# Optimization experiments

Hardware: AMD Instinct MI355X
Metric: run time of the kernel (lower is better)

Reference implementation:

```python
import jax, jax.numpy as jnp
import numpy as np

N_NODES = 50000


def sage_conv(x, src, dst, W_l, W_r, b):
    # mean-aggregate neighbor features: out_i = W_l @ mean_{j->i} x_j + W_r @ x_i + b
    msg_sum = jax.ops.segment_sum(x[src], dst, num_segments=N_NODES)   # [N, F]
    cnt = jax.ops.segment_sum(jnp.ones_like(dst, dtype=x.dtype), dst, num_segments=N_NODES)
    mean = msg_sum / jnp.maximum(cnt, 1.0)[:, None]                    # zero for isolated nodes
    return mean @ W_l + x @ W_r + b


def setup_inputs() -> dict:
    key = jax.random.key(0)
    ks = jax.random.split(key, 8)
    in_dim, hid, out_dim = 128, 128, 128
    x = jax.random.normal(ks[0], (N_NODES, in_dim), dtype=jnp.float32)
    edge_index = jax.random.randint(ks[1], (2, 800000), 0, N_NODES, dtype=jnp.int64)
    s0 = 1.0 / np.sqrt(in_dim)
    s1 = 1.0 / np.sqrt(hid)
    return {
        "x": x,
        "edge_index": edge_index,
        "W_l0": jax.random.uniform(ks[2], (in_dim, hid), jnp.float32, -s0, s0),
        "W_r0": jax.random.uniform(ks[3], (in_dim, hid), jnp.float32, -s0, s0),
        "b0": jnp.zeros((hid,), jnp.float32),
        "W_l1": jax.random.uniform(ks[4], (hid, out_dim), jnp.float32, -s1, s1),
        "W_r1": jax.random.uniform(ks[5], (hid, out_dim), jnp.float32, -s1, s1),
        "b1": jnp.zeros((out_dim,), jnp.float32),
    }


def reference(x, edge_index, W_l0, W_r0, b0, W_l1, W_r1, b1):
    src, dst = edge_index[0], edge_index[1]
    h = sage_conv(x, src, dst, W_l0, W_r0, b0)
    h = jax.nn.relu(h)
    out = sage_conv(h, src, dst, W_l1, W_r1, b1)
    return out
```

## Files before the change

### kernel.cpp

```cpp
#include <hip/hip_runtime.h>

#define FDIM 128
#define NGRP 8

typedef __attribute__((ext_vector_type(4))) float f32x4;
typedef __attribute__((ext_vector_type(8))) short s16x8;
typedef __attribute__((ext_vector_type(4))) short s16x4;

__device__ inline unsigned short f2bf(float f) {
    unsigned u = __builtin_bit_cast(unsigned, f);
    u += 0x7FFFu + ((u >> 16) & 1u);
    return (unsigned short)(u >> 16);
}
__device__ inline float bflo(unsigned u) { return __builtin_bit_cast(float, u << 16); }
__device__ inline float bfhi(unsigned u) { return __builtin_bit_cast(float, u & 0xFFFF0000u); }

__global__ void prologue_kernel(int4* __restrict__ degg4, int nz,
                                const float* __restrict__ x, short* __restrict__ xb, int n4x,
                                const float* __restrict__ Wl0, const float* __restrict__ Wr0,
                                const float* __restrict__ Wl1, const float* __restrict__ Wr1,
                                short* __restrict__ Wt0, short* __restrict__ Wt1,
                                int ZB, int XB) {
    int bid = blockIdx.x;
    if (bid < ZB) {
        int i = bid * 256 + threadIdx.x;
        if (i < nz) degg4[i] = make_int4(0, 0, 0, 0);
    } else if (bid < ZB + XB) {
        int i = (bid - ZB) * 256 + threadIdx.x;
        if (i < n4x) {
            float4 v = reinterpret_cast<const float4*>(x)[i];
            s16x4 o;
            o[0] = (short)f2bf(v.x); o[1] = (short)f2bf(v.y);
            o[2] = (short)f2bf(v.z); o[3] = (short)f2bf(v.w);
            reinterpret_cast<s16x4*>(xb)[i] = o;
        }
    } else {
        int g = (bid - ZB - XB) * 256 + threadIdx.x;
        int n = g & 127;
        int k = (g >> 7) & 255;
        int layer = g >> 15;
        const float* Wl = layer ? Wl1 : Wl0;
        const float* Wr = layer ? Wr1 : Wr0;
        short* Wt = layer ? Wt1 : Wt0;
        float v = (k < 128) ? Wl[k * 128 + n] : Wr[(k - 128) * 128 + n];
        Wt[n * 256 + k] = (short)f2bf(v);
    }
}

__global__ void hist8_kernel(const int* __restrict__ dst, int* __restrict__ degg, int E, int N) {
    int e = blockIdx.x * blockDim.x + threadIdx.x;
    if (e < E) atomicAdd(&degg[(blockIdx.x & 7) * N + dst[e]], 1);
}

__global__ void scanA1_kernel(const int* __restrict__ in, int* __restrict__ out,
                              int* __restrict__ bsum, int M) {
    __shared__ int s[256];
    int base = blockIdx.x * 1024 + threadIdx.x * 4;
    int4 v = make_int4(0, 0, 0, 0);
    if (base + 3 < M) v = *reinterpret_cast<const int4*>(in + base);
    else {
        if (base + 0 < M) v.x = in[base + 0];
        if (base + 1 < M) v.y = in[base + 1];
        if (base + 2 < M) v.z = in[base + 2];
        if (base + 3 < M) v.w = in[base + 3];
    }
    int tsum = v.x + v.y + v.z + v.w;
    s[threadIdx.x] = tsum;
    __syncthreads();
    for (int off = 1; off < 256; off <<= 1) {
        int t = (threadIdx.x >= off) ? s[threadIdx.x - off] : 0;
        __syncthreads();
        s[threadIdx.x] += t;
        __syncthreads();
    }
    int excl = s[threadIdx.x] - tsum;
    int4 o;
    o.x = excl; o.y = excl + v.x; o.z = o.y + v.y; o.w = o.z + v.z;
    if (base + 3 < M) *reinterpret_cast<int4*>(out + base) = o;
    else {
        if (base + 0 < M) out[base + 0] = o.x;
        if (base + 1 < M) out[base + 1] = o.y;
        if (base + 2 < M) out[base + 2] = o.z;
    }
    if (threadIdx.x == 255) bsum[blockIdx.x] = s[255];
}

__global__ void scanA3_kernel(int* __restrict__ off, int* __restrict__ cursor,
                              const int* __restrict__ bsum, int nb, int M, int E) {
    __shared__ int s[256];
    int t = threadIdx.x;
    int v = 0;
    if (t < blockIdx.x) v += bsum[t];
    if (t + 256 < blockIdx.x) v += bsum[t + 256];
    s[t] = v;
    __syncthreads();
    for (int off2 = 128; off2 > 0; off2 >>= 1) {
        if (t < off2) s[t] += s[t + off2];
        __syncthreads();
    }
    int b = s[0];

    int base = blockIdx.x * 1024 + t * 4;
    if (base + 3 < M) {
        int4 w = *reinterpret_cast<const int4*>(off + base);
        w.x += b; w.y += b; w.z += b; w.w += b;
        *reinterpret_cast<int4*>(off + base) = w;
        *reinterpret_cast<int4*>(cursor + base) = w;
    } else {
#pragma unroll
        for (int j = 0; j < 4; ++j)
            if (base + j < M) { int q = off[base + j] + b; off[base + j] = q; cursor[base + j] = q; }
    }
    if (base == 0) off[M] = E;
}

__global__ void rp_kernel(const int* __restrict__ off, int* __restrict__ rp, int N, int E) {
    __shared__ int S0;
    if (threadIdx.x == 0) {
        int s = 0;
#pragma unroll
        for (int g = 0; g < NGRP; ++g) s += off[g * N];
        S0 = s;
    }
    __syncthreads();
    int i = blockIdx.x * 256 + threadIdx.x;
    if (i < N) {
        int s = 0;
#pragma unroll
        for (int g = 0; g < NGRP; ++g) s += off[g * N + i];
        rp[i] = s - S0;
    } else if (i == N) {
        rp[N] = E;
    }
}

__global__ void fill8_kernel(const int* __restrict__ src, const int* __restrict__ dst,
                             int* __restrict__ cursor, int* __restrict__ eidt, int E, int N) {
    int e = blockIdx.x * blockDim.x + threadIdx.x;
    if (e < E) {
        int p = atomicAdd(&cursor[(blockIdx.x & 7) * N + dst[e]], 1);
        eidt[p] = src[e];
    }
}

__global__ void merge_kernel(const int* __restrict__ off, const int* __restrict__ eidt,
                             const int* __restrict__ rp, int* __restrict__ eid, int N) {
    int i = blockIdx.x * 256 + threadIdx.x;
    if (i >= N) return;
    int dp = rp[i];
#pragma unroll
    for (int g = 0; g < NGRP; ++g) {
        int b = off[g * N + i];
        int e2 = off[g * N + i + 1];
        for (int k = b; k < e2; ++k) eid[dp++] = eidt[k];
    }
}

#define ACC8(v) { a[0]+=bflo(v.x); a[1]+=bfhi(v.x); a[2]+=bflo(v.y); a[3]+=bfhi(v.y); \
                  a[4]+=bflo(v.z); a[5]+=bfhi(v.z); a[6]+=bflo(v.w); a[7]+=bfhi(v.w); }

__global__ void gather_kernel(const short* __restrict__ X, const int* __restrict__ rp,
                              const int* __restrict__ eid, short* __restrict__ mb, int N) {
    int node = blockIdx.x * (blockDim.x >> 6) + (threadIdx.x >> 6);
    int lane = threadIdx.x & 63;
    int g = lane >> 4;
    int c = lane & 15;
    if (node >= N) return;
    int beg = rp[node], end = rp[node + 1];
    float a[8];
#pragma unroll
    for (int j = 0; j < 8; ++j) a[j] = 0.0f;

    int k = beg;
    for (; k + 16 <= end; k += 16) {
        int s0 = eid[k + g];
        int s1 = eid[k + 4 + g];
        int s2 = eid[k + 8 + g];
        int s3 = eid[k + 12 + g];
        uint4 v0 = *reinterpret_cast<const uint4*>(X + (size_t)s0 * FDIM + c * 8);
        uint4 v1 = *reinterpret_cast<const uint4*>(X + (size_t)s1 * FDIM + c * 8);
        uint4 v2 = *reinterpret_cast<const uint4*>(X + (size_t)s2 * FDIM + c * 8);
        uint4 v3 = *reinterpret_cast<const uint4*>(X + (size_t)s3 * FDIM + c * 8);
        ACC8(v0); ACC8(v1); ACC8(v2); ACC8(v3);
    }
    if (k + 8 <= end) {
        int s0 = eid[k + g];
        int s1 = eid[k + 4 + g];
        uint4 v0 = *reinterpret_cast<const uint4*>(X + (size_t)s0 * FDIM + c * 8);
        uint4 v1 = *reinterpret_cast<const uint4*>(X + (size_t)s1 * FDIM + c * 8);
        ACC8(v0); ACC8(v1);
        k += 8;
    }
    if (k + 4 <= end) {
        int s0 = eid[k + g];
        uint4 v0 = *reinterpret_cast<const uint4*>(X + (size_t)s0 * FDIM + c * 8);
        ACC8(v0);
        k += 4;
    }
    int rem = end - k;
    if (g < rem) {
        int s0 = eid[k + g];
        uint4 v0 = *reinterpret_cast<const uint4*>(X + (size_t)s0 * FDIM + c * 8);
        ACC8(v0);
    }

#pragma unroll
    for (int j = 0; j < 8; ++j) a[j] += __shfl_xor(a[j], 16);
#pragma unroll
    for (int j = 0; j < 8; ++j) a[j] += __shfl_xor(a[j], 32);

    if (g == 0) {
        float inv = (end > beg) ? 1.0f / (float)(end - beg) : 0.0f;
        uint4 o;
        o.x = (unsigned)f2bf(a[0] * inv) | ((unsigned)f2bf(a[1] * inv) << 16);
        o.y = (unsigned)f2bf(a[2] * inv) | ((unsigned)f2bf(a[3] * inv) << 16);
        o.z = (unsigned)f2bf(a[4] * inv) | ((unsigned)f2bf(a[5] * inv) << 16);
        o.w = (unsigned)f2bf(a[6] * inv) | ((unsigned)f2bf(a[7] * inv) << 16);
        *reinterpret_cast<uint4*>(mb + (size_t)node * FDIM + c * 8) = o;
    }
}

template <bool RELU, bool OUTF32>
__global__ __launch_bounds__(256, 3)
void gemm_mfma_kernel(const short* __restrict__ Am, const short* Ax,
                      const short* __restrict__ Wt, const float* __restrict__ bias,
                      float* outf, short* outb, int n) {
    __shared__ short A_lds[64 * 256];
    const int tid = threadIdx.x;
    const int w = tid >> 6, l = tid & 63;
    const int row0 = blockIdx.x * 64;

    s16x8 bfr[8][2];
    {
        const short* wb = Wt + ((32 * w + (l & 15)) * 256 + 8 * (l >> 4));
#pragma unroll
        for (int kc = 0; kc < 8; ++kc)
#pragma unroll
            for (int cf = 0; cf < 2; ++cf)
                bfr[kc][cf] = *reinterpret_cast<const s16x8*>(wb + cf * 16 * 256 + kc * 32);
    }

#pragma unroll
    for (int i = 0; i < 8; ++i) {
        int c = tid + 256 * i;
        int r = c >> 5;
        int ck = c & 31;
        int row = row0 + r;
        s16x8 v;
        if (row < n) {
            const short* sp = (ck < 16) ? (Am + (size_t)row * FDIM + ck * 8)
                                        : (Ax + (size_t)row * FDIM + (ck - 16) * 8);
            v = *reinterpret_cast<const s16x8*>(sp);
        } else {
#pragma unroll
            for (int j = 0; j < 8; ++j) v[j] = 0;
        }
        int byte = r * 512 + ((ck * 16) ^ ((r & 7) << 4));
        *reinterpret_cast<s16x8*>(reinterpret_cast<char*>(A_lds) + byte) = v;
    }
    __syncthreads();

    f32x4 acc[4][2];
    {
        float b0 = bias[32 * w + (l & 15)];
        float b1 = bias[32 * w + 16 + (l & 15)];
#pragma unroll
        for (int rf = 0; rf < 4; ++rf)
#pragma unroll
            for (int i = 0; i < 4; ++i) { acc[rf][0][i] = b0; acc[rf][1][i] = b1; }
    }

    const int arow = l & 15;
    const int aq16 = 16 * (l >> 4);
#pragma unroll
    for (int kc = 0; kc < 8; ++kc) {
        s16x8 afr[4];
#pragma unroll
        for (int rf = 0; rf < 4; ++rf) {
            int r = 16 * rf + arow;
            int kbyte = 64 * kc + aq16;
            int byte = r * 512 + (kbyte ^ ((r & 7) << 4));
            afr[rf] = *reinterpret_cast<const s16x8*>(reinterpret_cast<const char*>(A_lds) + byte);
        }
#pragma unroll
        for (int rf = 0; rf < 4; ++rf)
#pragma unroll
            for (int cf = 0; cf < 2; ++cf)
                acc[rf][cf] = __builtin_amdgcn_mfma_f32_16x16x32_bf16(afr[rf], bfr[kc][cf], acc[rf][cf], 0, 0, 0);
    }

    const int ocol = 32 * w + (l & 15);
    const int orow = 4 * (l >> 4);
#pragma unroll
    for (int rf = 0; rf < 4; ++rf)
#pragma unroll
        for (int cf = 0; cf < 2; ++cf)
#pragma unroll
            for (int i = 0; i < 4; ++i) {
                int row = row0 + 16 * rf + orow + i;
                if (row < n) {
                    float v = acc[rf][cf][i];
                    if (RELU) v = fmaxf(v, 0.0f);
                    if (OUTF32) outf[(size_t)row * FDIM + ocol + 16 * cf] = v;
                    else        outb[(size_t)row * FDIM + ocol + 16 * cf] = (short)f2bf(v);
                }
            }
}

__global__ void degree_kernel(const int* __restrict__ dst, float* __restrict__ cnt, int E) {
    int e = blockIdx.x * blockDim.x + threadIdx.x;
    if (e < E) atomicAdd(&cnt[dst[e]], 1.0f);
}

__global__ void scatter_kernel(const float* __restrict__ x, const int* __restrict__ src,
                               const int* __restrict__ dst, float* __restrict__ msg, int E) {
    int gt = blockIdx.x * blockDim.x + threadIdx.x;
    int e = gt >> 6;
    int lane = gt & 63;
    if (e >= E) return;
    int s = src[e];
    int d = dst[e];
    float2 v = reinterpret_cast<const float2*>(x + (size_t)s * FDIM)[lane];
    float* md = msg + (size_t)d * FDIM + 2 * lane;
    atomicAdd(md, v.x);
    atomicAdd(md + 1, v.y);
}

template <bool RELU>
__global__ void gemm_kernel(const float* agg, const float* cnt,
                            const float* __restrict__ xin, const float* __restrict__ Wl,
                            const float* __restrict__ Wr, const float* __restrict__ bias,
                            float* out, int n) {
    const int ROWS = 16;
    __shared__ float m_s[ROWS][FDIM];
    __shared__ float x_s[ROWS][FDIM];
    int tid = threadIdx.x;
    int row0 = blockIdx.x * ROWS;
#pragma unroll
    for (int i = 0; i < 2; ++i) {
        int idx4 = tid + i * 256;
        int r = idx4 >> 5;
        int c4 = idx4 & 31;
        int row = row0 + r;
        if (row < n) {
            float inv = cnt ? 1.0f / fmaxf(cnt[row], 1.0f) : 1.0f;
            float4 mv = reinterpret_cast<const float4*>(agg + (size_t)row * FDIM)[c4];
            float4 xv = reinterpret_cast<const float4*>(xin + (size_t)row * FDIM)[c4];
            float* mp = &m_s[r][c4 * 4];
            mp[0] = mv.x * inv; mp[1] = mv.y * inv; mp[2] = mv.z * inv; mp[3] = mv.w * inv;
            float* xp = &x_s[r][c4 * 4];
            xp[0] = xv.x; xp[1] = xv.y; xp[2] = xv.z; xp[3] = xv.w;
        }
    }
    __syncthreads();
    int j = tid & 127;
    int rh = tid >> 7;
    float acc[8];
    float bj = bias[j];
#pragma unroll
    for (int r = 0; r < 8; ++r) acc[r] = bj;
#pragma unroll 4
    for (int k = 0; k < FDIM; ++k) {
        float wl = Wl[k * FDIM + j];
        float wr = Wr[k * FDIM + j];
#pragma unroll
        for (int r = 0; r < 8; ++r)
            acc[r] += m_s[rh * 8 + r][k] * wl + x_s[rh * 8 + r][k] * wr;
    }
#pragma unroll
    for (int r = 0; r < 8; ++r) {
        int row = row0 + rh * 8 + r;
        if (row < n) {
            float v = acc[r];
            if (RELU) v = fmaxf(v, 0.0f);
            out[(size_t)row * FDIM + j] = v;
        }
    }
}

extern "C" void kernel_launch(void* const* d_in, const int* in_sizes, int n_in,
                              void* d_out, int out_size, void* d_ws, size_t ws_size,
                              hipStream_t stream) {
    const float* x   = (const float*)d_in[0];
    const int*   ei  = (const int*)d_in[1];
    const float* Wl0 = (const float*)d_in[2];
    const float* Wr0 = (const float*)d_in[3];
    const float* b0  = (const float*)d_in[4];
    const float* Wl1 = (const float*)d_in[5];
    const float* Wr1 = (const float*)d_in[6];
    const float* b1  = (const float*)d_in[7];

    int N = in_sizes[0] / FDIM;
    int E = in_sizes[1] / 2;
    const int* src = ei;
    const int* dst = ei + E;

    size_t featBytes  = (size_t)N * FDIM * sizeof(float);
    size_t featBytesB = (size_t)N * FDIM * sizeof(short);
    int edgeBlocks = (E + 255) / 256;
    int M = NGRP * N;
    int blocksA = (M + 1023) / 1024;

    const size_t o_bsum = 0x0;
    const size_t o_rp   = 0x1000;
    const size_t o_wt0  = 0x33000;
    const size_t o_wt1  = 0x43000;
    const size_t o_eid  = 0x53000;
    const size_t o_xb   = 0x361000;
    const size_t o_mb   = o_xb + featBytesB;
    const size_t need   = o_mb + featBytesB;
    const size_t s_degg = o_mb + 0x0;
    const size_t s_off  = o_mb + 0x187000;
    const size_t s_cur  = o_mb + 0x30E000;
    const size_t s_eidt = o_mb + 0x495000;

    if (ws_size >= need && blocksA <= 512) {
        int*   bsum   = (int*)((char*)d_ws + o_bsum);
        int*   rp     = (int*)((char*)d_ws + o_rp);
        short* Wt0    = (short*)((char*)d_ws + o_wt0);
        short* Wt1    = (short*)((char*)d_ws + o_wt1);
        int*   eid    = (int*)((char*)d_ws + o_eid);
        short* xb     = (short*)((char*)d_ws + o_xb);
        short* mb     = (short*)((char*)d_ws + o_mb);
        int*   degg   = (int*)((char*)d_ws + s_degg);
        int*   off    = (int*)((char*)d_ws + s_off);
        int*   cursor = (int*)((char*)d_ws + s_cur);
        int*   eidt   = (int*)((char*)d_ws + s_eidt);
        float* outF   = (float*)d_out;

        int nz  = M / 4;
        int n4x = N * FDIM / 4;
        int ZB = (nz + 255) / 256;
        int XB = (n4x + 255) / 256;
        int WB = (65536 + 255) / 256;
        prologue_kernel<<<ZB + XB + WB, 256, 0, stream>>>(
            (int4*)degg, nz, x, xb, n4x, Wl0, Wr0, Wl1, Wr1, Wt0, Wt1, ZB, XB);

        hist8_kernel<<<edgeBlocks, 256, 0, stream>>>(dst, degg, E, N);
        scanA1_kernel<<<blocksA, 256, 0, stream>>>(degg, off, bsum, M);
        scanA3_kernel<<<blocksA, 256, 0, stream>>>(off, cursor, bsum, blocksA, M, E);
        rp_kernel<<<(N + 256) / 256, 256, 0, stream>>>(off, rp, N, E);
        fill8_kernel<<<edgeBlocks, 256, 0, stream>>>(src, dst, cursor, eidt, E, N);
        merge_kernel<<<(N + 255) / 256, 256, 0, stream>>>(off, eidt, rp, eid, N);

        int gatherBlocks = (N + 3) / 4;
        int gemmBlocks   = (N + 63) / 64;
        gather_kernel<<<gatherBlocks, 256, 0, stream>>>(xb, rp, eid, mb, N);
        gemm_mfma_kernel<true, false><<<gemmBlocks, 256, 0, stream>>>(mb, xb, Wt0, b0, nullptr, xb, N);
        gather_kernel<<<gatherBlocks, 256, 0, stream>>>(xb, rp, eid, mb, N);
        gemm_mfma_kernel<false, true><<<gemmBlocks, 256, 0, stream>>>(mb, xb, Wt1, b1, outF, nullptr, N);
    } else {
        float* cnt = (float*)d_ws;
        float* h   = (float*)((char*)d_ws + (1 << 18));
        float* msg = (float*)d_out;
        int gemmBlocks = (N + 15) / 16;

        hipMemsetAsync(cnt, 0, (size_t)N * sizeof(float), stream);
        degree_kernel<<<edgeBlocks, 256, 0, stream>>>(dst, cnt, E);

        hipMemsetAsync(msg, 0, featBytes, stream);
        scatter_kernel<<<(E * 64 + 255) / 256, 256, 0, stream>>>(x, src, dst, msg, E);
        gemm_kernel<true><<<gemmBlocks, 256, 0, stream>>>(msg, cnt, x, Wl0, Wr0, b0, h, N);

        hipMemsetAsync(msg, 0, featBytes, stream);
        scatter_kernel<<<(E * 64 + 255) / 256, 256, 0, stream>>>(h, src, dst, msg, E);
        gemm_kernel<false><<<gemmBlocks, 256, 0, stream>>>(msg, cnt, h, Wl1, Wr1, b1, msg, N);
    }
}
```

Before: 188.5 us.

## Fuse CSR build into fewer launches with a decoupled look-back single-pass scan

Replaces the two-pass block scan (scanA1 + scanA3) with a single-pass decoupled look-back scan that uses per-block status flags in the workspace. It folds the row-pointer computation into the merge kernel, and co-schedules the weight transpose with the histogram and the x-to-bf16 conversion with the fill kernel. This cuts the launch count in the preprocessing chain and lets independent work overlap the atomic-bound kernels. The look-back spins on flags and assumes earlier blocks make forward progress; the zero kernel must also clear the state array.

```diff
diff --git a/kernel.cpp b/kernel.cpp
--- a/kernel.cpp
+++ b/kernel.cpp
@@ -15,27 +15,21 @@
 __device__ inline float bflo(unsigned u) { return __builtin_bit_cast(float, u << 16); }
 __device__ inline float bfhi(unsigned u) { return __builtin_bit_cast(float, u & 0xFFFF0000u); }
 
-__global__ void prologue_kernel(int4* __restrict__ degg4, int nz,
-                                const float* __restrict__ x, short* __restrict__ xb, int n4x,
-                                const float* __restrict__ Wl0, const float* __restrict__ Wr0,
-                                const float* __restrict__ Wl1, const float* __restrict__ Wr1,
-                                short* __restrict__ Wt0, short* __restrict__ Wt1,
-                                int ZB, int XB) {
+__global__ void zero_kernel(int4* __restrict__ p, int n4) {
+    int i = blockIdx.x * blockDim.x + threadIdx.x;
+    if (i < n4) p[i] = make_int4(0, 0, 0, 0);
+}
+
+__global__ void hist8w_kernel(const int* __restrict__ dst, int* __restrict__ degg, int E, int N, int EB,
+                              const float* __restrict__ Wl0, const float* __restrict__ Wr0,
+                              const float* __restrict__ Wl1, const float* __restrict__ Wr1,
+                              short* __restrict__ Wt0, short* __restrict__ Wt1) {
     int bid = blockIdx.x;
-    if (bid < ZB) {
-        int i = bid * 256 + threadIdx.x;
-        if (i < nz) degg4[i] = make_int4(0, 0, 0, 0);
-    } else if (bid < ZB + XB) {
-        int i = (bid - ZB) * 256 + threadIdx.x;
-        if (i < n4x) {
-            float4 v = reinterpret_cast<const float4*>(x)[i];
-            s16x4 o;
-            o[0] = (short)f2bf(v.x); o[1] = (short)f2bf(v.y);
-            o[2] = (short)f2bf(v.z); o[3] = (short)f2bf(v.w);
-            reinterpret_cast<s16x4*>(xb)[i] = o;
-        }
+    if (bid < EB) {
+        int e = bid * 256 + threadIdx.x;
+        if (e < E) atomicAdd(&degg[(bid & 7) * N + dst[e]], 1);
     } else {
-        int g = (bid - ZB - XB) * 256 + threadIdx.x;
+        int g = (bid - EB) * 256 + threadIdx.x;
         int n = g & 127;
         int k = (g >> 7) & 255;
         int layer = g >> 15;
@@ -47,74 +41,112 @@
     }
 }
 
-__global__ void hist8_kernel(const int* __restrict__ dst, int* __restrict__ degg, int E, int N) {
-    int e = blockIdx.x * blockDim.x + threadIdx.x;
-    if (e < E) atomicAdd(&degg[(blockIdx.x & 7) * N + dst[e]], 1);
-}
-
-__global__ void scanA1_kernel(const int* __restrict__ in, int* __restrict__ out,
-                              int* __restrict__ bsum, int M) {
+__global__ __launch_bounds__(256)
+void scan_kernel(const int* __restrict__ in, int* __restrict__ out, int* __restrict__ cursor,
+                 unsigned* __restrict__ state, int M, int E) {
     __shared__ int s[256];
-    int base = blockIdx.x * 1024 + threadIdx.x * 4;
+    __shared__ int s_excl;
+    const int bid = blockIdx.x;
+    const int t = threadIdx.x;
+    int base = bid * 1024 + t * 4;
     int4 v = make_int4(0, 0, 0, 0);
     if (base + 3 < M) v = *reinterpret_cast<const int4*>(in + base);
     else {
         if (base + 0 < M) v.x = in[base + 0];
         if (base + 1 < M) v.y = in[base + 1];
         if (base + 2 < M) v.z = in[base + 2];
-        if (base + 3 < M) v.w = in[base + 3];
     }
     int tsum = v.x + v.y + v.z + v.w;
-    s[threadIdx.x] = tsum;
+    s[t] = tsum;
     __syncthreads();
-    for (int off = 1; off < 256; off <<= 1) {
-        int t = (threadIdx.x >= off) ? s[threadIdx.x - off] : 0;
+    for (int o2 = 1; o2 < 256; o2 <<= 1) {
+        int tt = (t >= o2) ? s[t - o2] : 0;
         __syncthreads();
-        s[threadIdx.x] += t;
+        s[t] += tt;
         __syncthreads();
     }
-    int excl = s[threadIdx.x] - tsum;
+    int total = s[255];
+    int texcl = s[t] - tsum;
+
+    if (t == 0) {
+        unsigned w = ((bid == 0 ? 2u : 1u) << 30) | (unsigned)total;
+        __hip_atomic_store(&state[bid], w, __ATOMIC_RELEASE, __HIP_MEMORY_SCOPE_AGENT);
+    }
+    if (t < 64) {
+        int excl = 0;
+        int j = bid - 1;
+        while (j >= 0) {
+            int idx = j - t;
+            unsigned w = 0;
+            if (idx >= 0) {
+                do {
+                    w = __hip_atomic_load(&state[idx], __ATOMIC_ACQUIRE, __HIP_MEMORY_SCOPE_AGENT);
+                } while ((w >> 30) == 0u);
+            }
+            int val = (int)(w & 0x3FFFFFFFu);
+            bool isPre = (idx >= 0) && ((w >> 30) == 2u);
+            unsigned long long mask = __ballot(isPre);
+            int contrib;
+            if (mask) {
+                int stop = __ffsll((unsigned long long)mask) - 1;
+                contrib = (t <= stop) ? val : 0;
+            } else {
+                contrib = (idx >= 0) ? val : 0;
+            }
+            for (int o = 32; o > 0; o >>= 1) contrib += __shfl_down(contrib, o);
+            excl += contrib;
+            if (mask) break;
+            j -= 64;
+        }
+        if (t == 0) {
+            s_excl = excl;
+            unsigned w = (2u << 30) | (unsigned)(excl + total);
+            __hip_atomic_store(&state[bid], w, __ATOMIC_RELEASE, __HIP_MEMORY_SCOPE_AGENT);
+        }
+    }
+    __syncthreads();
+    int b = s_excl;
+
+    int e0 = b + texcl;
     int4 o;
-    o.x = excl; o.y = excl + v.x; o.z = o.y + v.y; o.w = o.z + v.z;
-    if (base + 3 < M) *reinterpret_cast<int4*>(out + base) = o;
-    else {
-        if (base + 0 < M) out[base + 0] = o.x;
-        if (base + 1 < M) out[base + 1] = o.y;
-        if (base + 2 < M) out[base + 2] = o.z;
-    }
-    if (threadIdx.x == 255) bsum[blockIdx.x] = s[255];
-}
-
-__global__ void scanA3_kernel(int* __restrict__ off, int* __restrict__ cursor,
-                              const int* __restrict__ bsum, int nb, int M, int E) {
-    __shared__ int s[256];
-    int t = threadIdx.x;
-    int v = 0;
-    if (t < blockIdx.x) v += bsum[t];
-    if (t + 256 < blockIdx.x) v += bsum[t + 256];
-    s[t] = v;
-    __syncthreads();
-    for (int off2 = 128; off2 > 0; off2 >>= 1) {
-        if (t < off2) s[t] += s[t + off2];
-        __syncthreads();
-    }
-    int b = s[0];
-
-    int base = blockIdx.x * 1024 + t * 4;
+    o.x = e0; o.y = o.x + v.x; o.z = o.y + v.y; o.w = o.z + v.z;
     if (base + 3 < M) {
-        int4 w = *reinterpret_cast<const int4*>(off + base);
-        w.x += b; w.y += b; w.z += b; w.w += b;
-        *reinterpret_cast<int4*>(off + base) = w;
-        *reinterpret_cast<int4*>(cursor + base) = w;
+        *reinterpret_cast<int4*>(out + base) = o;
+        *reinterpret_cast<int4*>(cursor + base) = o;
     } else {
 #pragma unroll
-        for (int j = 0; j < 4; ++j)
-            if (base + j < M) { int q = off[base + j] + b; off[base + j] = q; cursor[base + j] = q; }
-    }
-    if (base == 0) off[M] = E;
-}
-
-__global__ void rp_kernel(const int* __restrict__ off, int* __restrict__ rp, int N, int E) {
+        for (int j2 = 0; j2 < 3; ++j2) {
+            int vv = (j2 == 0) ? o.x : (j2 == 1) ? o.y : o.z;
+            if (base + j2 < M) { out[base + j2] = vv; cursor[base + j2] = vv; }
+        }
+    }
+    if (bid == 0 && t == 0) out[M] = E;
+}
+
+__global__ void fill8x_kernel(const int* __restrict__ src, const int* __restrict__ dst,
+                              int* __restrict__ cursor, int* __restrict__ eidt, int E, int N, int EB,
+                              const float* __restrict__ x, short* __restrict__ xb, int n4x) {
+    int bid = blockIdx.x;
+    if (bid < EB) {
+        int e = bid * 256 + threadIdx.x;
+        if (e < E) {
+            int p = atomicAdd(&cursor[(bid & 7) * N + dst[e]], 1);
+            eidt[p] = src[e];
+        }
+    } else {
+        int i = (bid - EB) * 256 + threadIdx.x;
+        if (i < n4x) {
+            float4 v = reinterpret_cast<const float4*>(x)[i];
+            s16x4 o;
+            o[0] = (short)f2bf(v.x); o[1] = (short)f2bf(v.y);
+            o[2] = (short)f2bf(v.z); o[3] = (short)f2bf(v.w);
+            reinterpret_cast<s16x4*>(xb)[i] = o;
+        }
+    }
+}
+
+__global__ void merge_kernel(const int* __restrict__ off, const int* __restrict__ eidt,
+                             int* __restrict__ rp, int* __restrict__ eid, int N, int E) {
     __shared__ int S0;
     if (threadIdx.x == 0) {
         int s = 0;
@@ -124,36 +156,21 @@
     }
     __syncthreads();
     int i = blockIdx.x * 256 + threadIdx.x;
-    if (i < N) {
-        int s = 0;
-#pragma unroll
-        for (int g = 0; g < NGRP; ++g) s += off[g * N + i];
-        rp[i] = s - S0;
-    } else if (i == N) {
-        rp[N] = E;
-    }
-}
-
-__global__ void fill8_kernel(const int* __restrict__ src, const int* __restrict__ dst,
-                             int* __restrict__ cursor, int* __restrict__ eidt, int E, int N) {
-    int e = blockIdx.x * blockDim.x + threadIdx.x;
-    if (e < E) {
-        int p = atomicAdd(&cursor[(blockIdx.x & 7) * N + dst[e]], 1);
-        eidt[p] = src[e];
-    }
-}
-
-__global__ void merge_kernel(const int* __restrict__ off, const int* __restrict__ eidt,
-                             const int* __restrict__ rp, int* __restrict__ eid, int N) {
-    int i = blockIdx.x * 256 + threadIdx.x;
-    if (i >= N) return;
-    int dp = rp[i];
+    if (i > N) return;
+    if (i == N) { rp[N] = E; return; }
+    int bs[NGRP], es[NGRP];
+    int si = 0;
 #pragma unroll
     for (int g = 0; g < NGRP; ++g) {
-        int b = off[g * N + i];
-        int e2 = off[g * N + i + 1];
-        for (int k = b; k < e2; ++k) eid[dp++] = eidt[k];
-    }
+        bs[g] = off[g * N + i];
+        es[g] = off[g * N + i + 1];
+        si += bs[g];
+    }
+    int dp = si - S0;
+    rp[i] = dp;
+#pragma unroll
+    for (int g = 0; g < NGRP; ++g)
+        for (int k = bs[g]; k < es[g]; ++k) eid[dp++] = eidt[k];
 }
 
 #define ACC8(v) { a[0]+=bflo(v.x); a[1]+=bfhi(v.x); a[2]+=bflo(v.y); a[3]+=bfhi(v.y); \
@@ -401,7 +418,6 @@
     int M = NGRP * N;
     int blocksA = (M + 1023) / 1024;
 
-    const size_t o_bsum = 0x0;
     const size_t o_rp   = 0x1000;
     const size_t o_wt0  = 0x33000;
     const size_t o_wt1  = 0x43000;
@@ -409,39 +425,38 @@
     const size_t o_xb   = 0x361000;
     const size_t o_mb   = o_xb + featBytesB;
     const size_t need   = o_mb + featBytesB;
-    const size_t s_degg = o_mb + 0x0;
-    const size_t s_off  = o_mb + 0x187000;
-    const size_t s_cur  = o_mb + 0x30E000;
-    const size_t s_eidt = o_mb + 0x495000;
-
-    if (ws_size >= need && blocksA <= 512) {
-        int*   bsum   = (int*)((char*)d_ws + o_bsum);
-        int*   rp     = (int*)((char*)d_ws + o_rp);
-        short* Wt0    = (short*)((char*)d_ws + o_wt0);
-        short* Wt1    = (short*)((char*)d_ws + o_wt1);
-        int*   eid    = (int*)((char*)d_ws + o_eid);
-        short* xb     = (short*)((char*)d_ws + o_xb);
-        short* mb     = (short*)((char*)d_ws + o_mb);
-        int*   degg   = (int*)((char*)d_ws + s_degg);
-        int*   off    = (int*)((char*)d_ws + s_off);
-        int*   cursor = (int*)((char*)d_ws + s_cur);
-        int*   eidt   = (int*)((char*)d_ws + s_eidt);
-        float* outF   = (float*)d_out;
-
-        int nz  = M / 4;
+    const size_t s_degg  = o_mb + 0x0;
+    const size_t s_state = o_mb + 0x187000;
+    const size_t s_off   = o_mb + 0x18B000;
+    const size_t s_cur   = o_mb + 0x312000;
+    const size_t s_eidt  = o_mb + 0x499000;
+
+    if (ws_size >= need) {
+        int*      rp     = (int*)((char*)d_ws + o_rp);
+        short*    Wt0    = (short*)((char*)d_ws + o_wt0);
+        short*    Wt1    = (short*)((char*)d_ws + o_wt1);
+        int*      eid    = (int*)((char*)d_ws + o_eid);
+        short*    xb     = (short*)((char*)d_ws + o_xb);
+        short*    mb     = (short*)((char*)d_ws + o_mb);
+        int*      degg   = (int*)((char*)d_ws + s_degg);
+        unsigned* state  = (unsigned*)((char*)d_ws + s_state);
+        int*      off    = (int*)((char*)d_ws + s_off);
+        int*      cursor = (int*)((char*)d_ws + s_cur);
+        int*      eidt   = (int*)((char*)d_ws + s_eidt);
+        float*    outF   = (float*)d_out;
+
         int n4x = N * FDIM / 4;
-        int ZB = (nz + 255) / 256;
-        int XB = (n4x + 255) / 256;
-        int WB = (65536 + 255) / 256;
-        prologue_kernel<<<ZB + XB + WB, 256, 0, stream>>>(
-            (int4*)degg, nz, x, xb, n4x, Wl0, Wr0, Wl1, Wr1, Wt0, Wt1, ZB, XB);
-
-        hist8_kernel<<<edgeBlocks, 256, 0, stream>>>(dst, degg, E, N);
-        scanA1_kernel<<<blocksA, 256, 0, stream>>>(degg, off, bsum, M);
-        scanA3_kernel<<<blocksA, 256, 0, stream>>>(off, cursor, bsum, blocksA, M, E);
-        rp_kernel<<<(N + 256) / 256, 256, 0, stream>>>(off, rp, N, E);
-        fill8_kernel<<<edgeBlocks, 256, 0, stream>>>(src, dst, cursor, eidt, E, N);
-        merge_kernel<<<(N + 255) / 256, 256, 0, stream>>>(off, eidt, rp, eid, N);
+        int XB  = (n4x + 255) / 256;
+        int WB  = 256;
+        int nz  = 0x18B000 / 16;
+
+        zero_kernel<<<(nz + 255) / 256, 256, 0, stream>>>((int4*)degg, nz);
+        hist8w_kernel<<<edgeBlocks + WB, 256, 0, stream>>>(dst, degg, E, N, edgeBlocks,
+                                                           Wl0, Wr0, Wl1, Wr1, Wt0, Wt1);
+        scan_kernel<<<blocksA, 256, 0, stream>>>(degg, off, cursor, state, M, E);
+        fill8x_kernel<<<edgeBlocks + XB, 256, 0, stream>>>(src, dst, cursor, eidt, E, N, edgeBlocks,
+                                                           x, xb, n4x);
+        merge_kernel<<<(N + 1 + 255) / 256, 256, 0, stream>>>(off, eidt, rp, eid, N, E);
 
         int gatherBlocks = (N + 3) / 4;
         int gemmBlocks   = (N + 63) / 64;
```

After: 205.2 us. 8.9% more time.
